# Kernel optimization log

Hardware: AMD Instinct MI355X
Metric: run time of the kernel (lower is better)

The kernel has to match this reference:

```python
import jax, jax.numpy as jnp
import numpy as np

B, T, C = 2, 1024, 1024
H = 16
HD = C // H
S = 512   # short_term_memory_size
L = 1024  # sum(long_term_memory_size)
THETA = 10000.0


def setup_inputs() -> dict:
    key = jax.random.key(0)
    ks = jax.random.split(key, 7)
    return {
        "x": jax.random.normal(ks[0], (B, T, C), jnp.float32),
        "short_term_memory": jax.random.normal(ks[1], (B, S, C), jnp.float32),
        "long_q": jax.random.normal(ks[2], (B, L, H, HD), jnp.float32),
        "long_k": jax.random.normal(ks[3], (B, L, H, HD), jnp.float32),
        "long_v": jax.random.normal(ks[4], (B, L, H, HD), jnp.float32),
        "w_attn": jax.random.normal(ks[5], (C, 3 * C), jnp.float32) * 0.02,
        "w_proj": jax.random.normal(ks[6], (C, C), jnp.float32) * 0.02,
    }


def _rope_cos_sin(seq_len, dim, theta):
    # llama-style precompute_freqs_cis: freqs over even indices, angles = t * freq
    inv = 1.0 / (theta ** (jnp.arange(0, dim, 2, dtype=jnp.float32) / dim))
    t = jnp.arange(seq_len, dtype=jnp.float32)
    ang = jnp.outer(t, inv)  # [seq, dim//2]
    return jnp.cos(ang), jnp.sin(ang)


def _apply_rope(x, cos, sin):
    # x: [B, seq, H, hd] viewed as interleaved complex pairs (llama apply_rotary_emb)
    xr = x.reshape(*x.shape[:-1], HD // 2, 2)
    x0, x1 = xr[..., 0], xr[..., 1]
    c = cos[None, :, None, :]
    s = sin[None, :, None, :]
    o0 = x0 * c - x1 * s
    o1 = x0 * s + x1 * c
    return jnp.stack([o0, o1], axis=-1).reshape(x.shape)


def _memory_mask():
    # create_memory_mask: tril over M=L+S+T, rows [L, L+S) fully visible
    M = L + S + T
    m = np.tril(np.ones((M, M), dtype=np.float32))
    m[L:L + S, :] = 1.0
    return jnp.asarray(m)


_MASK = _memory_mask()


def reference(x, short_term_memory, long_q, long_k, long_v, w_attn, w_proj):
    # prepend short-term memory tokens, project qkv
    xcat = jnp.concatenate([short_term_memory, x], axis=1)          # [B, S+T, C]
    qkv = xcat @ w_attn                                             # [B, S+T, 3C]
    q, k, v = jnp.split(qkv, 3, axis=-1)
    q = q.reshape(B, S + T, H, HD)
    k = k.reshape(B, S + T, H, HD)
    v = v.reshape(B, S + T, H, HD)
    # in-place rotary on the last S+T positions (long-term part untouched)
    cos, sin = _rope_cos_sin(S + T, HD, THETA)
    q = _apply_rope(q, cos, sin)
    k = _apply_rope(k, cos, sin)
    # concat pre-rotated long-term memory in front
    q = jnp.concatenate([long_q, q], axis=1)                        # [B, M, H, hd]
    k = jnp.concatenate([long_k, k], axis=1)
    v = jnp.concatenate([long_v, v], axis=1)
    q, k, v = (t.transpose(0, 2, 1, 3) for t in (q, k, v))          # [B, H, M, hd]
    att = jnp.einsum('bhqd,bhkd->bhqk', q, k) * (1.0 / jnp.sqrt(jnp.float32(HD)))
    att = jnp.where(_MASK == 0, -jnp.inf, att)
    att = jax.nn.softmax(att, axis=-1)
    y = jnp.einsum('bhqk,bhkd->bhqd', att, v)                       # [B, H, M, hd]
    y = y.transpose(0, 2, 1, 3).reshape(B, L + S + T, C)
    y = y[:, -T:, :] @ w_proj                                       # [B, T, C]
    return y
```

## Files before the change

### kernel.cpp

```cpp
#include <hip/hip_runtime.h>
#include <math.h>

#define BB 2
#define TT 1024
#define CC 1024
#define HH 16
#define HD 64
#define SS 512
#define LL 1024
#define ST 1536
#define MM 2560
#define C3 3072

typedef __attribute__((ext_vector_type(8))) short short8;
typedef __attribute__((ext_vector_type(4))) short short4v;
typedef __attribute__((ext_vector_type(4))) float floatx4;

__device__ __forceinline__ unsigned short f2bf(float f) {
    union { float f; unsigned u; } v; v.f = f;
    unsigned r = v.u + 0x7fffu + ((v.u >> 16) & 1u);
    return (unsigned short)(r >> 16);
}
__device__ __forceinline__ float bf2f(short s) {
    union { unsigned u; float f; } v;
    v.u = ((unsigned)(unsigned short)s) << 16;
    return v.f;
}

__device__ __forceinline__ void gl_lds16(const short* g, short* l) {
    __builtin_amdgcn_global_load_lds(
        (const __attribute__((address_space(1))) void*)g,
        (__attribute__((address_space(3))) void*)l,
        16, 0, 0);
}

__global__ __launch_bounds__(256)
void prep_all(const float* __restrict__ x, const float* __restrict__ stm,
              const float* __restrict__ w_attn, const float* __restrict__ w_proj,
              const float* __restrict__ lk, const float* __restrict__ lv,
              short* __restrict__ Xb, short* __restrict__ WaT,
              short* __restrict__ WpT, short* __restrict__ Kg,
              short* __restrict__ Vt, float* __restrict__ tab)
{
    __shared__ __align__(16) char smem[9216];
    const int blk = blockIdx.x;
    const int t = threadIdx.x;

    if (blk < 3072) {
        const int idx = blk * 256 + t;
        const int rg  = idx >> 8;
        const int c   = (idx & 255) << 2;
        const int b   = rg >= ST;
        const int r   = rg - b * ST;
        const float* src = (r < SS) ? (stm + ((size_t)b * SS + r) * CC + c)
                                    : (x   + ((size_t)b * TT + (r - SS)) * CC + c);
        float4 v = *(const float4*)src;
        short4v o;
        o.x = (short)f2bf(v.x); o.y = (short)f2bf(v.y);
        o.z = (short)f2bf(v.z); o.w = (short)f2bf(v.w);
        *(short4v*)(Xb + (size_t)rg * CC + c) = o;
    } else if (blk < 7168) {
        const bool isA = blk < 6144;
        const int bx = isA ? (blk - 3072) : (blk - 6144);
        const int nblk = isA ? 96 : 32;
        const int Nd = isA ? C3 : CC;
        const float* W = isA ? w_attn : w_proj;
        short* WT = isA ? WaT : WpT;
        const int n0 = (bx % nblk) * 32, k0 = (bx / nblk) * 32;
        float (*Tl)[33] = (float(*)[33])smem;
        const int r = t >> 3, c4 = (t & 7) << 2;
        float4 v = *(const float4*)(W + (size_t)(k0 + r) * Nd + n0 + c4);
        Tl[r][c4 + 0] = v.x; Tl[r][c4 + 1] = v.y;
        Tl[r][c4 + 2] = v.z; Tl[r][c4 + 3] = v.w;
        __syncthreads();
        short4v o;
        o.x = (short)f2bf(Tl[c4 + 0][r]); o.y = (short)f2bf(Tl[c4 + 1][r]);
        o.z = (short)f2bf(Tl[c4 + 2][r]); o.w = (short)f2bf(Tl[c4 + 3][r]);
        *(short4v*)(WT + (size_t)(n0 + r) * CC + k0 + c4) = o;
    } else if (blk < 7360) {
        const int idx = (blk - 7168) * 256 + t;
        const int r = idx >> 5, e = idx & 31;
        const float inv = powf(10000.0f, -(float)e * (1.0f / 32.0f));
        float sn, cs;
        sincosf((float)r * inv, &sn, &cs);
        tab[idx * 2] = cs;
        tab[idx * 2 + 1] = sn;
    } else {
        const int bx = blk - 7360;
        const int bh = bx >> 4, j0 = (bx & 15) * 64;
        const int b = bh >> 4, h = bh & 15;
        short (*Tl)[72] = (short(*)[72])smem;
        const int jr = t >> 2, c16 = (t & 3) << 4;
        const size_t si = (((size_t)b * LL + j0 + jr) * HH + h) * HD + c16;
        short kk[16], vv[16];
        #pragma unroll
        for (int u = 0; u < 4; u++) {
            float4 kv = *(const float4*)(lk + si + 4 * u);
            float4 vf = *(const float4*)(lv + si + 4 * u);
            kk[4*u+0] = (short)f2bf(kv.x); kk[4*u+1] = (short)f2bf(kv.y);
            kk[4*u+2] = (short)f2bf(kv.z); kk[4*u+3] = (short)f2bf(kv.w);
            vv[4*u+0] = (short)f2bf(vf.x); vv[4*u+1] = (short)f2bf(vf.y);
            vv[4*u+2] = (short)f2bf(vf.z); vv[4*u+3] = (short)f2bf(vf.w);
        }
        short* kdst = Kg + ((size_t)bh * MM + j0 + jr) * HD + c16;
        *(short8*)kdst       = *(short8*)&kk[0];
        *(short8*)(kdst + 8) = *(short8*)&kk[8];
        #pragma unroll
        for (int u = 0; u < 16; u++) Tl[jr][c16 + u] = vv[u];
        __syncthreads();
        const int r = t >> 2, c = t & 3;
        short o0[8], o1[8];
        #pragma unroll
        for (int u = 0; u < 8; u++) {
            o0[u] = Tl[c * 16 + u][r];
            o1[u] = Tl[c * 16 + 8 + u][r];
        }
        short* vdst = Vt + ((size_t)bh * HD + r) * MM + j0 + c * 16;
        *(short8*)vdst       = *(short8*)&o0[0];
        *(short8*)(vdst + 8) = *(short8*)&o1[0];
    }
}

__global__ __launch_bounds__(256)
void qkv_gemm(const short* __restrict__ A, const short* __restrict__ Bt,
              const float* __restrict__ RT,
              short* __restrict__ Qo, short* __restrict__ Ko, short* __restrict__ Vo)
{
    __shared__ short As[128 * 32];
    __shared__ short Bs[128 * 32];
    __shared__ short Et[128 * 132];
    const int b = blockIdx.z;
    const int row0 = blockIdx.y * 128, col0 = blockIdx.x * 128;
    const int tid = threadIdx.x;
    const int w = tid >> 6, l = tid & 63, quad = l >> 4, cl = l & 15;
    const int wr = w >> 1, wc = w & 1;

    const int reg  = col0 >> 10;
    const bool hasQ = (row0 >= SS);
    if (reg == 0 && !hasQ) return;

    const int srow = (l >> 2);
    const int schunk = ((l & 3) - (srow >> 1)) & 3;
    const int arow = w * 32 + srow;
    const short* gA0 = A + ((size_t)b * ST + row0 + arow) * CC + schunk * 8;
    const short* gA1 = gA0 + (size_t)16 * CC;
    const short* gB0 = Bt + (size_t)(col0 + arow) * CC + schunk * 8;
    const short* gB1 = gB0 + (size_t)16 * CC;
    short* lA0 = &As[(w * 32) * 32 + l * 8];
    short* lA1 = &As[(w * 32 + 16) * 32 + l * 8];
    short* lB0 = &Bs[(w * 32) * 32 + l * 8];
    short* lB1 = &Bs[(w * 32 + 16) * 32 + l * 8];

    const int fs = (quad + (cl >> 1)) & 3;

    floatx4 acc[4][4];
    #pragma unroll
    for (int mi = 0; mi < 4; mi++)
        #pragma unroll
        for (int ni = 0; ni < 4; ni++) acc[mi][ni] = (floatx4){0.f, 0.f, 0.f, 0.f};

    for (int k0 = 0; k0 < CC; k0 += 32) {
        __syncthreads();
        gl_lds16(gA0 + k0, lA0);
        gl_lds16(gA1 + k0, lA1);
        gl_lds16(gB0 + k0, lB0);
        gl_lds16(gB1 + k0, lB1);
        __syncthreads();
        short8 af[4], bf[4];
        #pragma unroll
        for (int mi = 0; mi < 4; mi++)
            af[mi] = *(const short8*)&As[(wr * 64 + mi * 16 + cl) * 32 + fs * 8];
        #pragma unroll
        for (int ni = 0; ni < 4; ni++)
            bf[ni] = *(const short8*)&Bs[(wc * 64 + ni * 16 + cl) * 32 + fs * 8];
        #pragma unroll
        for (int mi = 0; mi < 4; mi++)
            #pragma unroll
            for (int ni = 0; ni < 4; ni++)
                acc[mi][ni] = __builtin_amdgcn_mfma_f32_16x16x32_bf16(
                    af[mi], bf[ni], acc[mi][ni], 0, 0, 0);
    }

    #pragma unroll
    for (int ni = 0; ni < 4; ni++) {
        const int c_local = wc * 64 + ni * 16 + cl;
        const int e = (c_local & 63) >> 1;
        #pragma unroll
        for (int mi = 0; mi < 4; mi++) {
            #pragma unroll
            for (int r = 0; r < 4; r++) {
                const int R_local = wr * 64 + mi * 16 + quad * 4 + r;
                const int R = row0 + R_local;
                float v = acc[mi][ni][r];
                if (reg < 2) {
                    const float2 tt = ((const float2*)RT)[R * 32 + e];
                    float po = __shfl_xor(v, 1);
                    float out = ((cl & 1) == 0) ? (v * tt.x - po * tt.y)
                                                : (po * tt.y + v * tt.x);
                    unsigned short bfv = f2bf(out);
                    int ob = __shfl_xor((int)bfv, 1);
                    if ((cl & 1) == 0) {
                        unsigned word = (unsigned)bfv | (((unsigned)ob & 0xffffu) << 16);
                        *(unsigned*)&Et[R_local * 132 + c_local] = word;
                    }
                } else {
                    Et[c_local * 132 + R_local] = (short)f2bf(v);
                }
            }
        }
    }
    __syncthreads();

    const int hh0 = (col0 & 1023) >> 6;
    if (reg < 2) {
        #pragma unroll
        for (int hf = 0; hf < 2; hf++) {
            const int hh = hh0 + hf;
            short* dstb = (reg == 0)
                ? Qo + (((size_t)b * HH + hh) * TT + (row0 - SS)) * HD
                : Ko + (((size_t)b * HH + hh) * MM + LL + row0) * HD;
            #pragma unroll
            for (int it = 0; it < 4; it++) {
                const int idx = it * 2048 + tid * 8;
                const int r = idx >> 6, d = idx & 63;
                short4v v0 = *(const short4v*)&Et[r * 132 + hf * 64 + d];
                short4v v1 = *(const short4v*)&Et[r * 132 + hf * 64 + d + 4];
                short8 vv;
                #pragma unroll
                for (int u = 0; u < 4; u++) { vv[u] = v0[u]; vv[u + 4] = v1[u]; }
                *(short8*)(dstb + idx) = vv;
            }
        }
    } else {
        #pragma unroll
        for (int it = 0; it < 8; it++) {
            const int idx = it * 2048 + tid * 8;
            const int c = idx >> 7, r0 = idx & 127;
            const int hh = hh0 + (c >> 6), d = c & 63;
            short4v v0 = *(const short4v*)&Et[c * 132 + r0];
            short4v v1 = *(const short4v*)&Et[c * 132 + r0 + 4];
            short8 vv;
            #pragma unroll
            for (int u = 0; u < 4; u++) { vv[u] = v0[u]; vv[u + 4] = v1[u]; }
            *(short8*)(Vo + (((size_t)b * HH + hh) * HD + d) * MM + LL + row0 + r0) = vv;
        }
    }
}

#define PSP 72
#define PSW (32 * PSP)
#define VS_OFF 4096
#define PS_OFF 8192
__global__ __launch_bounds__(256, 4)
void attn_mfma(const short* __restrict__ Qg, const short* __restrict__ Kg,
               const short* __restrict__ Vt, short* __restrict__ Op,
               float* __restrict__ Lp)
{
    __shared__ __align__(16) short L[17408];

    const int bh = blockIdx.x;
    const int q0 = (7 - blockIdx.y) * 128;
    const int piece = blockIdx.z;
    const int tid = threadIdx.x, w = tid >> 6, l = tid & 63;
    const int quad = l >> 4, cl = l & 15;

    short8 qa[2][2];
    #pragma unroll
    for (int g = 0; g < 2; g++) {
        const short* qptr = Qg + ((size_t)bh * TT + q0 + w * 32 + g * 16 + cl) * HD + quad * 8;
        qa[g][0] = *(const short8*)qptr;
        qa[g][1] = *(const short8*)(qptr + 32);
    }

    floatx4 o[2][4];
    float rs[2][4];
    #pragma unroll
    for (int g = 0; g < 2; g++)
        #pragma unroll
        for (int r = 0; r < 4; r++) {
            rs[g][r] = 0.f;
            o[g][r] = (floatx4){0.f, 0.f, 0.f, 0.f};
        }

    const int srow_lo = l >> 3;
    const int sslot  = l & 7;
    const int ch0 = (sslot - (srow_lo >> 1)) & 7;
    const int ch1 = (sslot - (4 + (srow_lo >> 1))) & 7;
    const int rowi0 = w * 16 + srow_lo;
    const int rowi1 = w * 16 + 8 + srow_lo;
    const short* kgb = Kg + (size_t)bh * MM * HD;
    const short* vbase = Vt + (size_t)bh * HD * MM;
    short* ldsK0 = &L[(w * 16) * 64];
    short* ldsK1 = &L[(w * 16 + 8) * 64];
    short* ldsV0 = &L[VS_OFF + (w * 16) * 64];
    short* ldsV1 = &L[VS_OFF + (w * 16 + 8) * 64];

    const int fsA = (quad + (cl >> 1)) & 7;
    const int fsB = (quad + 4 + (cl >> 1)) & 7;
    const int psA = (quad + 2 * cl) & 7;
    const int psB = (quad + 4 + 2 * cl) & 7;

    const int ntiles = (LL + SS + q0) / 64 + 2;
    const int t_begin = piece * ntiles / 4;
    const int t_end   = (piece + 1) * ntiles / 4;

    for (int t = t_begin; t < t_end; t++) {
        const int j0 = t * 64;
        __syncthreads();
        gl_lds16(kgb + (size_t)(j0 + rowi0) * HD + ch0 * 8, ldsK0);
        gl_lds16(kgb + (size_t)(j0 + rowi1) * HD + ch1 * 8, ldsK1);
        gl_lds16(vbase + (size_t)rowi0 * MM + j0 + ch0 * 8, ldsV0);
        gl_lds16(vbase + (size_t)rowi1 * MM + j0 + ch1 * 8, ldsV1);
        __syncthreads();

        floatx4 s[2][4];
        #pragma unroll
        for (int ks = 0; ks < 4; ks++) {
            const int krow = ks * 16 + cl;
            short8 kf0 = *(const short8*)&L[krow * 64 + fsA * 8];
            short8 kf1 = *(const short8*)&L[krow * 64 + fsB * 8];
            #pragma unroll
            for (int g = 0; g < 2; g++) {
                floatx4 z = (floatx4){0.f, 0.f, 0.f, 0.f};
                z = __builtin_amdgcn_mfma_f32_16x16x32_bf16(qa[g][0], kf0, z, 0, 0, 0);
                z = __builtin_amdgcn_mfma_f32_16x16x32_bf16(qa[g][1], kf1, z, 0, 0, 0);
                s[g][ks] = z;
            }
        }

        const bool tailzone = (t >= ntiles - 2);
        #pragma unroll
        for (int g = 0; g < 2; g++) {
            const int qgb = LL + SS + q0 + w * 32 + g * 16;
            #pragma unroll
            for (int ks = 0; ks < 4; ks++) {
                #pragma unroll
                for (int r = 0; r < 4; r++) {
                    float sv = s[g][ks][r] * 0.125f;
                    if (tailzone && (j0 + ks * 16 + cl > qgb + quad * 4 + r))
                        sv = -INFINITY;
                    const float p = __expf(sv);
                    rs[g][r] += p;
                    const int qrw = quad * 4 + r;
                    const int slot = (ks * 2 + (cl >> 3) + 2 * qrw) & 7;
                    L[PS_OFF + w * PSW + (g * 16 + qrw) * PSP + slot * 8 + (cl & 7)] =
                        (short)f2bf(p);
                }
            }
        }

        __builtin_amdgcn_s_waitcnt(0xc07f);
        __builtin_amdgcn_wave_barrier();

        short8 pf[2][2];
        #pragma unroll
        for (int g = 0; g < 2; g++) {
            pf[g][0] = *(const short8*)&L[PS_OFF + w * PSW + (g * 16 + cl) * PSP + psA * 8];
            pf[g][1] = *(const short8*)&L[PS_OFF + w * PSW + (g * 16 + cl) * PSP + psB * 8];
        }
        #pragma unroll
        for (int nt = 0; nt < 4; nt++) {
            const int drow = nt * 16 + cl;
            short8 vf0 = *(const short8*)&L[VS_OFF + drow * 64 + fsA * 8];
            short8 vf1 = *(const short8*)&L[VS_OFF + drow * 64 + fsB * 8];
            #pragma unroll
            for (int g = 0; g < 2; g++) {
                o[g][nt] = __builtin_amdgcn_mfma_f32_16x16x32_bf16(pf[g][0], vf0, o[g][nt], 0, 0, 0);
                o[g][nt] = __builtin_amdgcn_mfma_f32_16x16x32_bf16(pf[g][1], vf1, o[g][nt], 0, 0, 0);
            }
        }
    }

    #pragma unroll
    for (int g = 0; g < 2; g++)
        #pragma unroll
        for (int r = 0; r < 4; r++) {
            float t2 = rs[g][r];
            t2 += __shfl_xor(t2, 1);
            t2 += __shfl_xor(t2, 2);
            t2 += __shfl_xor(t2, 4);
            t2 += __shfl_xor(t2, 8);
            if (cl == 0)
                Lp[piece * 32768 + bh * 1024 + q0 + w * 32 + g * 16 + quad * 4 + r] = t2;
        }

    __syncthreads();
    #pragma unroll
    for (int g = 0; g < 2; g++)
        #pragma unroll
        for (int r = 0; r < 4; r++) {
            const int ql = w * 32 + g * 16 + quad * 4 + r;
            #pragma unroll
            for (int nt = 0; nt < 4; nt++)
                L[ql * 68 + nt * 16 + cl] = (short)f2bf(o[g][nt][r]);
        }
    __syncthreads();
    short* ob = Op + ((size_t)(piece * 32 + bh) * 1024 + q0) * 64;
    #pragma unroll
    for (int it = 0; it < 4; it++) {
        const int idx = it * 2048 + tid * 8;
        const int q = idx >> 6, d = idx & 63;
        short4v v0 = *(const short4v*)&L[q * 68 + d];
        short4v v1 = *(const short4v*)&L[q * 68 + d + 4];
        short8 vv;
        #pragma unroll
        for (int u = 0; u < 4; u++) { vv[u] = v0[u]; vv[u + 4] = v1[u]; }
        *(short8*)(ob + idx) = vv;
    }
}

__global__ __launch_bounds__(256)
void attn_combine(const short* __restrict__ Op, const float* __restrict__ Lp,
                  short* __restrict__ Yatt)
{
    const int idx = blockIdx.x * 256 + threadIdx.x;
    const int row = idx >> 3;
    const int seg = (idx & 7) << 3;
    const float lsum = Lp[row] + Lp[32768 + row] + Lp[65536 + row] + Lp[98304 + row];
    const float inv = 1.0f / lsum;
    float acc[8] = {0.f, 0.f, 0.f, 0.f, 0.f, 0.f, 0.f, 0.f};
    #pragma unroll
    for (int p = 0; p < 4; p++) {
        short8 v = *(const short8*)(Op + ((size_t)(p * 32768) + row) * 64 + seg);
        #pragma unroll
        for (int u = 0; u < 8; u++) acc[u] += bf2f(v[u]);
    }
    short8 o8;
    #pragma unroll
    for (int u = 0; u < 8; u++) o8[u] = (short)f2bf(acc[u] * inv);
    const int bh = row >> 10, q = row & 1023;
    const int b = bh >> 4, h = bh & 15;
    *(short8*)(Yatt + ((size_t)b * TT + q) * CC + h * 64 + seg) = o8;
}

__global__ __launch_bounds__(256)
void proj_gemm(const short* __restrict__ A, const short* __restrict__ Bt,
               float* __restrict__ Co)
{
    __shared__ short As[64 * 32];
    __shared__ short Bs[64 * 32];
    const int row0 = blockIdx.y * 64, col0 = blockIdx.x * 64;
    const int tid = threadIdx.x;
    const int w = tid >> 6, l = tid & 63, quad = l >> 4, cl = l & 15;
    const int wr = w >> 1, wc = w & 1;

    const int srow = tid >> 2;
    const int schunk = ((tid & 3) - ((srow & 15) >> 1)) & 3;
    const short* gA = A + (size_t)(row0 + srow) * CC + schunk * 8;
    const short* gB = Bt + (size_t)(col0 + srow) * CC + schunk * 8;
    short* lA = &As[tid * 8];
    short* lB = &Bs[tid * 8];

    const int fs = (quad + (cl >> 1)) & 3;

    floatx4 acc[2][2];
    #pragma unroll
    for (int mi = 0; mi < 2; mi++)
        #pragma unroll
        for (int ni = 0; ni < 2; ni++) acc[mi][ni] = (floatx4){0.f, 0.f, 0.f, 0.f};

    for (int k0 = 0; k0 < CC; k0 += 32) {
        __syncthreads();
        gl_lds16(gA + k0, lA);
        gl_lds16(gB + k0, lB);
        __syncthreads();
        short8 af[2], bf[2];
        #pragma unroll
        for (int mi = 0; mi < 2; mi++)
            af[mi] = *(const short8*)&As[(wr * 32 + mi * 16 + cl) * 32 + fs * 8];
        #pragma unroll
        for (int ni = 0; ni < 2; ni++)
            bf[ni] = *(const short8*)&Bs[(wc * 32 + ni * 16 + cl) * 32 + fs * 8];
        #pragma unroll
        for (int mi = 0; mi < 2; mi++)
            #pragma unroll
            for (int ni = 0; ni < 2; ni++)
                acc[mi][ni] = __builtin_amdgcn_mfma_f32_16x16x32_bf16(
                    af[mi], bf[ni], acc[mi][ni], 0, 0, 0);
    }
    #pragma unroll
    for (int mi = 0; mi < 2; mi++)
        #pragma unroll
        for (int ni = 0; ni < 2; ni++)
            #pragma unroll
            for (int r = 0; r < 4; r++)
                Co[(size_t)(row0 + wr * 32 + mi * 16 + quad * 4 + r) * CC
                   + col0 + wc * 32 + ni * 16 + cl] = acc[mi][ni][r];
}

extern "C" void kernel_launch(void* const* d_in, const int* in_sizes, int n_in,
                              void* d_out, int out_size, void* d_ws, size_t ws_size,
                              hipStream_t stream)
{
    (void)in_sizes; (void)n_in; (void)out_size; (void)ws_size;
    const float* x      = (const float*)d_in[0];
    const float* stm    = (const float*)d_in[1];
    const float* long_k = (const float*)d_in[3];
    const float* long_v = (const float*)d_in[4];
    const float* w_attn = (const float*)d_in[5];
    const float* w_proj = (const float*)d_in[6];
    float* out = (float*)d_out;

    short* Xb   = (short*)d_ws;
    short* WaT  = Xb   + (size_t)3145728;
    short* WpT  = WaT  + (size_t)3145728;
    short* Qb   = WpT  + (size_t)1048576;
    short* Kb   = Qb   + (size_t)2097152;
    short* Vtr  = Kb   + (size_t)5242880;
    short* Yb   = Vtr  + (size_t)5242880;
    float* RTab = (float*)(Yb + (size_t)2097152);
    short* Opart = (short*)(RTab + 98304);
    float* Lpart = (float*)(Opart + (size_t)8388608);

    prep_all<<<7872, 256, 0, stream>>>(x, stm, w_attn, w_proj, long_k, long_v,
                                       Xb, WaT, WpT, Kb, Vtr, RTab);

    qkv_gemm<<<dim3(24, 12, 2), 256, 0, stream>>>(Xb, WaT, RTab, Qb, Kb, Vtr);

    attn_mfma<<<dim3(32, 8, 4), 256, 0, stream>>>(Qb, Kb, Vtr, Opart, Lpart);
    attn_combine<<<1024, 256, 0, stream>>>(Opart, Lpart, Yb);

    proj_gemm<<<dim3(16, 32), 256, 0, stream>>>(Yb, WpT, out);
}
```

Baseline: 203.9 us.

## Double-buffer K/V tiles in attention kernel with async prefetch of next tile

The attention kernel now keeps two LDS buffers for K/V tiles and issues the global-to-LDS loads for tile t+1 before computing tile t, waiting with partial vmcnt so the loads overlap compute. It also splits the loop body into separate masked and unmasked tile variants, and packs pairs of probabilities into bf16x2 with a lane shuffle and v_cvt_pk_bf16_f32 so half the lanes write 32-bit LDS words. LDS use grows, so launch bounds drop from 4 to 3 blocks per CU, which lowers occupancy in exchange for the overlap.

```diff
diff --git a/kernel.cpp b/kernel.cpp
--- a/kernel.cpp
+++ b/kernel.cpp
@@ -249,14 +249,13 @@
 
 #define PSP 72
 #define PSW (32 * PSP)
-#define VS_OFF 4096
-#define PS_OFF 8192
-__global__ __launch_bounds__(256, 4)
+#define PS_OFF 16384
+__global__ __launch_bounds__(256, 3)
 void attn_mfma(const short* __restrict__ Qg, const short* __restrict__ Kg,
                const short* __restrict__ Vt, short* __restrict__ Op,
                float* __restrict__ Lp)
 {
-    __shared__ __align__(16) short L[17408];
+    __shared__ __align__(16) short L[25600];
 
     const int bh = blockIdx.x;
     const int q0 = (7 - blockIdx.y) * 128;
@@ -287,13 +286,9 @@
     const int ch0 = (sslot - (srow_lo >> 1)) & 7;
     const int ch1 = (sslot - (4 + (srow_lo >> 1))) & 7;
     const int rowi0 = w * 16 + srow_lo;
-    const int rowi1 = w * 16 + 8 + srow_lo;
+    const int rowi1 = rowi0 + 8;
     const short* kgb = Kg + (size_t)bh * MM * HD;
     const short* vbase = Vt + (size_t)bh * HD * MM;
-    short* ldsK0 = &L[(w * 16) * 64];
-    short* ldsK1 = &L[(w * 16 + 8) * 64];
-    short* ldsV0 = &L[VS_OFF + (w * 16) * 64];
-    short* ldsV1 = &L[VS_OFF + (w * 16 + 8) * 64];
 
     const int fsA = (quad + (cl >> 1)) & 7;
     const int fsB = (quad + 4 + (cl >> 1)) & 7;
@@ -303,73 +298,112 @@
     const int ntiles = (LL + SS + q0) / 64 + 2;
     const int t_begin = piece * ntiles / 4;
     const int t_end   = (piece + 1) * ntiles / 4;
-
+    const int t_tail  = ntiles - 2;
+
+#define STAGE(tt, bb) do {                                                    \
+    const int jj0 = (tt) * 64;                                                \
+    short* lk_ = &L[((bb) << 13) + (w << 10)];                                \
+    short* lv_ = lk_ + 4096;                                                  \
+    gl_lds16(kgb + (size_t)(jj0 + rowi0) * HD + ch0 * 8, lk_);                \
+    gl_lds16(kgb + (size_t)(jj0 + rowi1) * HD + ch1 * 8, lk_ + 512);          \
+    gl_lds16(vbase + (size_t)rowi0 * MM + jj0 + ch0 * 8, lv_);                \
+    gl_lds16(vbase + (size_t)rowi1 * MM + jj0 + ch1 * 8, lv_ + 512);          \
+} while (0)
+
+#define TILE(tt, kb_, TAILZONE) do {                                          \
+    const int jj0 = (tt) * 64; (void)jj0;                                     \
+    floatx4 s[2][4];                                                          \
+    _Pragma("unroll")                                                         \
+    for (int ks = 0; ks < 4; ks++) {                                          \
+        const int krow = ks * 16 + cl;                                        \
+        short8 kf0 = *(const short8*)&L[(kb_) + krow * 64 + fsA * 8];         \
+        short8 kf1 = *(const short8*)&L[(kb_) + krow * 64 + fsB * 8];         \
+        _Pragma("unroll")                                                     \
+        for (int g = 0; g < 2; g++) {                                         \
+            floatx4 z = (floatx4){0.f, 0.f, 0.f, 0.f};                        \
+            z = __builtin_amdgcn_mfma_f32_16x16x32_bf16(qa[g][0], kf0, z, 0, 0, 0); \
+            z = __builtin_amdgcn_mfma_f32_16x16x32_bf16(qa[g][1], kf1, z, 0, 0, 0); \
+            s[g][ks] = z;                                                     \
+        }                                                                     \
+    }                                                                         \
+    _Pragma("unroll")                                                         \
+    for (int g = 0; g < 2; g++) {                                             \
+        const int qgb = LL + SS + q0 + w * 32 + g * 16; (void)qgb;            \
+        unsigned pw[4][4];                                                    \
+        _Pragma("unroll")                                                     \
+        for (int ks = 0; ks < 4; ks++) {                                      \
+            _Pragma("unroll")                                                 \
+            for (int r = 0; r < 4; r++) {                                     \
+                float sv = s[g][ks][r] * 0.125f;                              \
+                if (TAILZONE) {                                               \
+                    if (jj0 + ks * 16 + cl > qgb + quad * 4 + r)              \
+                        sv = -INFINITY;                                       \
+                }                                                             \
+                const float p = __expf(sv);                                   \
+                rs[g][r] += p;                                                \
+                const float po = __shfl_xor(p, 1);                            \
+                unsigned w32;                                                 \
+                asm("v_cvt_pk_bf16_f32 %0, %1, %2"                            \
+                    : "=v"(w32) : "v"(p), "v"(po));                           \
+                pw[ks][r] = w32;                                              \
+            }                                                                 \
+        }                                                                     \
+        if ((cl & 1) == 0) {                                                  \
+            _Pragma("unroll")                                                 \
+            for (int ks = 0; ks < 4; ks++) {                                  \
+                _Pragma("unroll")                                             \
+                for (int r = 0; r < 4; r++) {                                 \
+                    const int qrw = quad * 4 + r;                             \
+                    const int slot = (ks * 2 + (cl >> 3) + 2 * qrw) & 7;      \
+                    *(unsigned*)&L[PS_OFF + w * PSW + (g * 16 + qrw) * PSP    \
+                                   + slot * 8 + (cl & 7)] = pw[ks][r];        \
+                }                                                             \
+            }                                                                 \
+        }                                                                     \
+    }                                                                         \
+    __builtin_amdgcn_s_waitcnt(0xc07f);       \
+    __builtin_amdgcn_wave_barrier();                                          \
+    short8 pf[2][2];                                                          \
+    _Pragma("unroll")                                                         \
+    for (int g = 0; g < 2; g++) {                                             \
+        pf[g][0] = *(const short8*)&L[PS_OFF + w * PSW + (g * 16 + cl) * PSP + psA * 8]; \
+        pf[g][1] = *(const short8*)&L[PS_OFF + w * PSW + (g * 16 + cl) * PSP + psB * 8]; \
+    }                                                                         \
+    _Pragma("unroll")                                                         \
+    for (int nt = 0; nt < 4; nt++) {                                          \
+        const int drow = nt * 16 + cl;                                        \
+        short8 vf0 = *(const short8*)&L[(kb_) + 4096 + drow * 64 + fsA * 8];  \
+        short8 vf1 = *(const short8*)&L[(kb_) + 4096 + drow * 64 + fsB * 8];  \
+        _Pragma("unroll")                                                     \
+        for (int g = 0; g < 2; g++) {                                         \
+            o[g][nt] = __builtin_amdgcn_mfma_f32_16x16x32_bf16(pf[g][0], vf0, o[g][nt], 0, 0, 0); \
+            o[g][nt] = __builtin_amdgcn_mfma_f32_16x16x32_bf16(pf[g][1], vf1, o[g][nt], 0, 0, 0); \
+        }                                                                     \
+    }                                                                         \
+} while (0)
+
+    int cur = 0;
+    if (t_begin < t_end) STAGE(t_begin, 0);
     for (int t = t_begin; t < t_end; t++) {
-        const int j0 = t * 64;
-        __syncthreads();
-        gl_lds16(kgb + (size_t)(j0 + rowi0) * HD + ch0 * 8, ldsK0);
-        gl_lds16(kgb + (size_t)(j0 + rowi1) * HD + ch1 * 8, ldsK1);
-        gl_lds16(vbase + (size_t)rowi0 * MM + j0 + ch0 * 8, ldsV0);
-        gl_lds16(vbase + (size_t)rowi1 * MM + j0 + ch1 * 8, ldsV1);
-        __syncthreads();
-
-        floatx4 s[2][4];
-        #pragma unroll
-        for (int ks = 0; ks < 4; ks++) {
-            const int krow = ks * 16 + cl;
-            short8 kf0 = *(const short8*)&L[krow * 64 + fsA * 8];
-            short8 kf1 = *(const short8*)&L[krow * 64 + fsB * 8];
-            #pragma unroll
-            for (int g = 0; g < 2; g++) {
-                floatx4 z = (floatx4){0.f, 0.f, 0.f, 0.f};
-                z = __builtin_amdgcn_mfma_f32_16x16x32_bf16(qa[g][0], kf0, z, 0, 0, 0);
-                z = __builtin_amdgcn_mfma_f32_16x16x32_bf16(qa[g][1], kf1, z, 0, 0, 0);
-                s[g][ks] = z;
-            }
-        }
-
-        const bool tailzone = (t >= ntiles - 2);
-        #pragma unroll
-        for (int g = 0; g < 2; g++) {
-            const int qgb = LL + SS + q0 + w * 32 + g * 16;
-            #pragma unroll
-            for (int ks = 0; ks < 4; ks++) {
-                #pragma unroll
-                for (int r = 0; r < 4; r++) {
-                    float sv = s[g][ks][r] * 0.125f;
-                    if (tailzone && (j0 + ks * 16 + cl > qgb + quad * 4 + r))
-                        sv = -INFINITY;
-                    const float p = __expf(sv);
-                    rs[g][r] += p;
-                    const int qrw = quad * 4 + r;
-                    const int slot = (ks * 2 + (cl >> 3) + 2 * qrw) & 7;
-                    L[PS_OFF + w * PSW + (g * 16 + qrw) * PSP + slot * 8 + (cl & 7)] =
-                        (short)f2bf(p);
-                }
-            }
-        }
-
+        const int nb = cur ^ 1;
+        if (t + 1 < t_end) {
+            STAGE(t + 1, nb);
+            __builtin_amdgcn_s_waitcnt(0x0F74);
+        } else {
+            __builtin_amdgcn_s_waitcnt(0x0F70);
+        }
+        __builtin_amdgcn_s_barrier();
+        __builtin_amdgcn_sched_barrier(0);
+        const int kb = cur << 13;
+        if (t < t_tail) { TILE(t, kb, 0); }
+        else            { TILE(t, kb, 1); }
         __builtin_amdgcn_s_waitcnt(0xc07f);
-        __builtin_amdgcn_wave_barrier();
-
-        short8 pf[2][2];
-        #pragma unroll
-        for (int g = 0; g < 2; g++) {
-            pf[g][0] = *(const short8*)&L[PS_OFF + w * PSW + (g * 16 + cl) * PSP + psA * 8];
-            pf[g][1] = *(const short8*)&L[PS_OFF + w * PSW + (g * 16 + cl) * PSP + psB * 8];
-        }
-        #pragma unroll
-        for (int nt = 0; nt < 4; nt++) {
-            const int drow = nt * 16 + cl;
-            short8 vf0 = *(const short8*)&L[VS_OFF + drow * 64 + fsA * 8];
-            short8 vf1 = *(const short8*)&L[VS_OFF + drow * 64 + fsB * 8];
-            #pragma unroll
-            for (int g = 0; g < 2; g++) {
-                o[g][nt] = __builtin_amdgcn_mfma_f32_16x16x32_bf16(pf[g][0], vf0, o[g][nt], 0, 0, 0);
-                o[g][nt] = __builtin_amdgcn_mfma_f32_16x16x32_bf16(pf[g][1], vf1, o[g][nt], 0, 0, 0);
-            }
-        }
-    }
+        __builtin_amdgcn_sched_barrier(0);
+        __builtin_amdgcn_s_barrier();
+        cur = nb;
+    }
+#undef STAGE
+#undef TILE
 
     #pragma unroll
     for (int g = 0; g < 2; g++)
```

Result: slower. 227.9 us (+11.8%).
